# Optimization experiments

Measured on AMD Instinct MI355X. Metric: run time of the kernel, lower is better.

The kernel has to match this reference:

```python
import jax, jax.numpy as jnp
import numpy as np

B, CIN, IMG = 2, 3, 128
E, NH, WS, L, HID = 256, 8, 8, 4, 1024
HD = E // NH
SCALE = HD ** -0.5
T = WS * WS  # tokens per window


def _layernorm(x, g, b):
    m = x.mean(-1, keepdims=True)
    v = ((x - m) ** 2).mean(-1, keepdims=True)
    return (x - m) * jax.lax.rsqrt(v + 1e-5) * g + b


def _build_mask(H, W, ws, ss):
    # Swin shifted-window mask, built with static numpy (H,W,ws,ss are static)
    img = np.zeros((H, W), np.float32)
    cnt = 0
    sl = lambda n: (slice(0, n - ws), slice(n - ws, n - ss), slice(n - ss, n))
    for h in sl(H):
        for w in sl(W):
            img[h, w] = cnt
            cnt += 1
    mw = img.reshape(H // ws, ws, W // ws, ws).transpose(0, 2, 1, 3).reshape(-1, ws * ws)
    d = mw[:, None, :] - mw[:, :, None]
    return jnp.asarray(np.where(d != 0, -100.0, 0.0).astype(np.float32))  # [nW,T,T]


def _win_attn(xseq, H, W, wqkv, bqkv, wproj, bproj, mask):
    Bn, N, C = xseq.shape
    nWh, nWw = H // WS, W // WS
    nW = nWh * nWw
    # window partition: [B,N,C] -> [B*nW, T, C]
    xw = xseq.reshape(Bn, nWh, WS, nWw, WS, C).transpose(0, 1, 3, 2, 4, 5).reshape(Bn * nW, T, C)
    qkv = (xw @ wqkv + bqkv).reshape(Bn * nW, T, 3, NH, HD).transpose(2, 0, 3, 1, 4)
    q, k, v = qkv[0], qkv[1], qkv[2]  # [B*nW, NH, T, HD]
    attn = jnp.einsum('whtd,whsd->whts', q, k) * SCALE
    if mask is not None:
        attn = (attn.reshape(Bn, nW, NH, T, T) + mask[None, :, None]).reshape(Bn * nW, NH, T, T)
    attn = jax.nn.softmax(attn, axis=-1)
    out = jnp.einsum('whts,whsd->wthd', attn, v).reshape(Bn * nW, T, C)
    out = out @ wproj + bproj
    # window merge
    out = out.reshape(Bn, nWh, nWw, WS, WS, C).transpose(0, 1, 3, 2, 4, 5).reshape(Bn, H * W, C)
    return out


def _forward(x, in_w, in_b, pos, ln1_g, ln1_b, qkv_w, qkv_b, proj_w, proj_b,
             ln2_g, ln2_b, mlp_w1, mlp_b1, mlp_w2, mlp_b2, out_w, out_b):
    Bx, _, H, W = x.shape
    ss = WS // 2
    y = jnp.einsum('bchw,ec->behw', x, in_w) + in_b[None, :, None, None] + pos
    seq = y.transpose(0, 2, 3, 1).reshape(Bx, H * W, E)
    mask = _build_mask(H, W, WS, ss)
    for i in range(L):
        shifted = (i % 2 == 1)
        if shifted:
            seq = jnp.roll(seq.reshape(Bx, H, W, E), (-ss, -ss), (1, 2)).reshape(Bx, H * W, E)
        h = _layernorm(seq, ln1_g[i], ln1_b[i])
        seq = seq + _win_attn(h, H, W, qkv_w[i], qkv_b[i], proj_w[i], proj_b[i],
                              mask if shifted else None)
        h = _layernorm(seq, ln2_g[i], ln2_b[i])
        seq = seq + (jax.nn.gelu(h @ mlp_w1[i] + mlp_b1[i], approximate=False) @ mlp_w2[i] + mlp_b2[i])
        if shifted:
            seq = jnp.roll(seq.reshape(Bx, H, W, E), (ss, ss), (1, 2)).reshape(Bx, H * W, E)
    out = seq.reshape(Bx, H, W, E).transpose(0, 3, 1, 2)
    return jnp.einsum('bchw,ec->behw', out, out_w) + out_b[None, :, None, None]


def setup_inputs() -> dict:
    key = jax.random.key(0)
    ks = jax.random.split(key, 10)
    std = jnp.float32(0.02)
    return {
        'x': jax.random.normal(ks[0], (B, CIN, IMG, IMG), jnp.float32),
        'in_w': jax.random.normal(ks[1], (E, CIN), jnp.float32) * std,
        'in_b': jnp.zeros((E,), jnp.float32),
        'pos': jax.random.normal(ks[2], (1, E, IMG, IMG), jnp.float32) * std,
        'ln1_g': jnp.ones((L, E), jnp.float32),
        'ln1_b': jnp.zeros((L, E), jnp.float32),
        'qkv_w': jax.random.normal(ks[3], (L, E, 3 * E), jnp.float32) * std,
        'qkv_b': jnp.zeros((L, 3 * E), jnp.float32),
        'proj_w': jax.random.normal(ks[4], (L, E, E), jnp.float32) * std,
        'proj_b': jnp.zeros((L, E), jnp.float32),
        'ln2_g': jnp.ones((L, E), jnp.float32),
        'ln2_b': jnp.zeros((L, E), jnp.float32),
        'mlp_w1': jax.random.normal(ks[5], (L, E, HID), jnp.float32) * std,
        'mlp_b1': jnp.zeros((L, HID), jnp.float32),
        'mlp_w2': jax.random.normal(ks[6], (L, HID, E), jnp.float32) * std,
        'mlp_b2': jnp.zeros((L, E), jnp.float32),
        'out_w': jax.random.normal(ks[7], (E, E), jnp.float32) * std,
        'out_b': jnp.zeros((E,), jnp.float32),
    }


def reference(x, in_w, in_b, pos, ln1_g, ln1_b, qkv_w, qkv_b, proj_w, proj_b,
              ln2_g, ln2_b, mlp_w1, mlp_b1, mlp_w2, mlp_b2, out_w, out_b):
    return _forward(x, in_w, in_b, pos, ln1_g, ln1_b, qkv_w, qkv_b, proj_w, proj_b,
                    ln2_g, ln2_b, mlp_w1, mlp_b1, mlp_w2, mlp_b2, out_w, out_b)
```

## Files before the change

kernel.cpp:

```cpp
#include <hip/hip_runtime.h>
#include <math.h>

#define E_DIM 256
#define NPB 16384
#define M_TOT 32768

typedef __attribute__((ext_vector_type(4))) float f32x4;
typedef __attribute__((ext_vector_type(8))) short s16x8;

__device__ inline unsigned short f2bu(float f) {
  union { float f; unsigned int i; } x; x.f = f;
  unsigned int r = x.i + 0x7fffu + ((x.i >> 16) & 1u);
  return (unsigned short)(r >> 16);
}
__device__ inline float bu2f(unsigned short u) {
  union { unsigned int i; float f; } x; x.i = ((unsigned int)u) << 16; return x.f;
}
__device__ inline void gload16(const void* g, void* l) {
  __builtin_amdgcn_global_load_lds(
      (const __attribute__((address_space(1))) void*)g,
      (__attribute__((address_space(3))) void*)l, 16, 0, 0);
}
__device__ inline float fgelu(float v) {
  float u2 = 2.0f * v * (0.7978845608f + 0.0356774081f * v * v);
  u2 = fminf(fmaxf(u2, -30.0f), 30.0f);
  float e = __expf(u2);
  return v * (e / (e + 1.0f));
}

__global__ __launch_bounds__(256) void embed_kernel(
    const float* __restrict__ x, const float* __restrict__ in_w,
    const float* __restrict__ in_b, const float* __restrict__ pos,
    float* __restrict__ seq)
{
  __shared__ float ld[32][33];
  int e0 = blockIdx.x * 32;
  int n0 = blockIdx.y * 32;
  int b  = n0 >> 14;
  int np = n0 & (NPB - 1);
  int tx = threadIdx.x & 31, ty = threadIdx.x >> 5;
  #pragma unroll
  for (int i = 0; i < 4; i++)
    ld[ty + 8*i][tx] = pos[(size_t)(e0 + ty + 8*i) * NPB + np + tx];
  __syncthreads();
  #pragma unroll
  for (int i = 0; i < 4; i++) {
    int n = np + ty + 8*i;
    float x0 = x[(b*3 + 0)*NPB + n];
    float x1 = x[(b*3 + 1)*NPB + n];
    float x2 = x[(b*3 + 2)*NPB + n];
    int e = e0 + tx;
    float v = x0*in_w[e*3+0] + x1*in_w[e*3+1] + x2*in_w[e*3+2] + in_b[e]
            + ld[tx][ty + 8*i];
    seq[(size_t)(n0 + ty + 8*i) * E_DIM + e] = v;
  }
}

__global__ __launch_bounds__(256) void ln_kernel(
    const float* __restrict__ x, const float* __restrict__ g,
    const float* __restrict__ b, unsigned short* __restrict__ y)
{
  int token = blockIdx.x * 4 + (threadIdx.x >> 6);
  int lane  = threadIdx.x & 63;
  const float4* xr = (const float4*)(x + (size_t)token * E_DIM);
  float4 v = xr[lane];
  float s = v.x + v.y + v.z + v.w;
  #pragma unroll
  for (int off = 32; off; off >>= 1) s += __shfl_xor(s, off);
  float mean = s * (1.0f / E_DIM);
  float d0 = v.x - mean, d1 = v.y - mean, d2 = v.z - mean, d3 = v.w - mean;
  float q = d0*d0 + d1*d1 + d2*d2 + d3*d3;
  #pragma unroll
  for (int off = 32; off; off >>= 1) q += __shfl_xor(q, off);
  float rstd = rsqrtf(q * (1.0f / E_DIM) + 1e-5f);
  float4 gg = ((const float4*)g)[lane];
  float4 bb = ((const float4*)b)[lane];
  ushort4 o;
  o.x = f2bu(d0 * rstd * gg.x + bb.x);
  o.y = f2bu(d1 * rstd * gg.y + bb.y);
  o.z = f2bu(d2 * rstd * gg.z + bb.z);
  o.w = f2bu(d3 * rstd * gg.w + bb.w);
  *(ushort4*)(y + (size_t)token * E_DIM + lane * 4) = o;
}

__global__ __launch_bounds__(256) void wconv_t(
    const float* __restrict__ W, unsigned short* __restrict__ Wt, int K, int N)
{
  __shared__ float t[32][33];
  int nb = blockIdx.x * 32, kb = blockIdx.y * 32;
  int tx = threadIdx.x & 31, ty = threadIdx.x >> 5;
  #pragma unroll
  for (int i = 0; i < 32; i += 8)
    t[ty + i][tx] = W[(size_t)(kb + ty + i) * N + nb + tx];
  __syncthreads();
  #pragma unroll
  for (int i = 0; i < 32; i += 8)
    Wt[(size_t)(nb + ty + i) * K + kb + tx] = f2bu(t[tx][ty + i]);
}

__global__ __launch_bounds__(256) void bconv(
    const float* __restrict__ a, unsigned short* __restrict__ o, int n)
{
  int i = blockIdx.x * 1024 + threadIdx.x * 4;
  float4 v = *(const float4*)(a + i);
  ushort4 u; u.x = f2bu(v.x); u.y = f2bu(v.y); u.z = f2bu(v.z); u.w = f2bu(v.w);
  *(ushort4*)(o + i) = u;
}

__device__ inline int rowf(int r) { return (r & 3) ^ ((r >> 2) & 3); }

template<int ACT, int OCHW, int OBF>
__global__ __launch_bounds__(512) void mgemm_a(
    const unsigned short* __restrict__ A, const unsigned short* __restrict__ Wt,
    const float* __restrict__ bias, void* __restrict__ Cv, int N, int K)
{
  __shared__ unsigned short Al[2][128 * 32];
  __shared__ unsigned short Bl[2][256 * 32];
  const int tid  = threadIdx.x;
  const int lane = tid & 63;
  const int wid  = tid >> 6;
  const int wr = wid >> 2, wc = wid & 3;
  const int nbx = N >> 8;
  const int bid = blockIdx.x;
  const int lt  = (bid & 7) * ((int)gridDim.x >> 3) + (bid >> 3);
  const int bn  = (lt % nbx) * 256, bm = (lt / nbx) * 128;

  f32x4 acc[4][4];
  #pragma unroll
  for (int m = 0; m < 4; m++)
    #pragma unroll
    for (int n = 0; n < 4; n++)
      acc[m][n] = (f32x4){0.f, 0.f, 0.f, 0.f};

  const int srow = tid >> 2;
  const int cs   = (tid & 3) ^ rowf(srow);
  const unsigned short* aSrc  = A  + (size_t)(bm + srow) * K + cs * 8;
  const unsigned short* bSrc0 = Wt + (size_t)(bn + srow) * K + cs * 8;
  const unsigned short* bSrc1 = Wt + (size_t)(bn + srow + 128) * K + cs * 8;

  const int slotx = (lane >> 4) ^ (lane & 3) ^ ((lane >> 2) & 3);
  const int aoff = (wr*64 + (lane & 15)) * 64 + slotx * 16;
  const int boff = (wc*64 + (lane & 15)) * 64 + slotx * 16;

  {
    gload16(aSrc,  (char*)Al[0] + tid * 16);
    gload16(bSrc0, (char*)Bl[0] + tid * 16);
    gload16(bSrc1, (char*)Bl[0] + tid * 16 + 8192);
  }
  __syncthreads();

  const int nt = K >> 5;
  int cur = 0;
  for (int t = 0; t < nt; ++t) {
    if (t + 1 < nt) {
      int k0 = (t + 1) << 5;
      gload16(aSrc + k0,  (char*)Al[cur ^ 1] + tid * 16);
      gload16(bSrc0 + k0, (char*)Bl[cur ^ 1] + tid * 16);
      gload16(bSrc1 + k0, (char*)Bl[cur ^ 1] + tid * 16 + 8192);
    }
    const char* ab = (const char*)Al[cur] + aoff;
    const char* bb = (const char*)Bl[cur] + boff;
    s16x8 af[4], bf_[4];
    #pragma unroll
    for (int m = 0; m < 4; m++) af[m]  = *(const s16x8*)(ab + m * 1024);
    #pragma unroll
    for (int n = 0; n < 4; n++) bf_[n] = *(const s16x8*)(bb + n * 1024);
    #pragma unroll
    for (int m = 0; m < 4; m++)
      #pragma unroll
      for (int n = 0; n < 4; n++)
        acc[m][n] = __builtin_amdgcn_mfma_f32_16x16x32_bf16(af[m], bf_[n], acc[m][n], 0, 0, 0);
    __syncthreads();
    cur ^= 1;
  }

  float bv[4];
  #pragma unroll
  for (int n = 0; n < 4; n++) bv[n] = bias[bn + wc*64 + n*16 + (lane & 15)];

  #pragma unroll
  for (int m = 0; m < 4; m++) {
    int row0 = bm + wr*64 + m*16 + (lane >> 4) * 4;
    #pragma unroll
    for (int n = 0; n < 4; n++) {
      int col = bn + wc*64 + n*16 + (lane & 15);
      if (OCHW) {
        int bb2 = row0 >> 14, n0 = row0 & (NPB - 1);
        float4 st;
        st.x = acc[m][n][0] + bv[n]; st.y = acc[m][n][1] + bv[n];
        st.z = acc[m][n][2] + bv[n]; st.w = acc[m][n][3] + bv[n];
        *(float4*)((float*)Cv + (size_t)bb2 * E_DIM * NPB + (size_t)col * NPB + n0) = st;
      } else {
        #pragma unroll
        for (int j = 0; j < 4; j++) {
          int row = row0 + j;
          float v = acc[m][n][j] + bv[n];
          if (ACT) v = fgelu(v);
          if (OBF) ((unsigned short*)Cv)[(size_t)row * N + col] = f2bu(v);
          else     ((float*)Cv)[(size_t)row * N + col] = v;
        }
      }
    }
  }
}

template<int LNC>
__global__ __launch_bounds__(512) void mgemm_res(
    const unsigned short* __restrict__ A, const unsigned short* __restrict__ Wt,
    const float* __restrict__ bias, float* __restrict__ seq,
    const float* __restrict__ gamma, const float* __restrict__ beta,
    unsigned short* __restrict__ hb, int K)
{
  __shared__ unsigned short Al[2][64 * 32];
  __shared__ unsigned short Bl[2][256 * 32];
  __shared__ float2 ws[64][4];
  const int tid  = threadIdx.x;
  const int lane = tid & 63;
  const int wid  = tid >> 6;
  const int wr = wid >> 2, wc = wid & 3;
  const int bid = blockIdx.x;
  const int lt  = (bid & 7) * ((int)gridDim.x >> 3) + (bid >> 3);
  const int bm  = lt * 64;

  f32x4 acc[2][4];
  #pragma unroll
  for (int m = 0; m < 2; m++)
    #pragma unroll
    for (int n = 0; n < 4; n++)
      acc[m][n] = (f32x4){0.f, 0.f, 0.f, 0.f};

  const int srow = tid >> 2;
  const int cs   = (tid & 3) ^ rowf(srow);
  const unsigned short* aSrc  = A  + (size_t)(bm + srow) * K + cs * 8;
  const unsigned short* bSrc0 = Wt + (size_t)srow * K + cs * 8;
  const unsigned short* bSrc1 = Wt + (size_t)(srow + 128) * K + cs * 8;

  const int slotx = (lane >> 4) ^ (lane & 3) ^ ((lane >> 2) & 3);
  const int aoff = (wr*32 + (lane & 15)) * 64 + slotx * 16;
  const int boff = (wc*64 + (lane & 15)) * 64 + slotx * 16;

  {
    if (tid < 256) gload16(aSrc, (char*)Al[0] + tid * 16);
    gload16(bSrc0, (char*)Bl[0] + tid * 16);
    gload16(bSrc1, (char*)Bl[0] + tid * 16 + 8192);
  }
  __syncthreads();

  const int nt = K >> 5;
  int cur = 0;
  for (int t = 0; t < nt; ++t) {
    if (t + 1 < nt) {
      int k0 = (t + 1) << 5;
      if (tid < 256) gload16(aSrc + k0, (char*)Al[cur ^ 1] + tid * 16);
      gload16(bSrc0 + k0, (char*)Bl[cur ^ 1] + tid * 16);
      gload16(bSrc1 + k0, (char*)Bl[cur ^ 1] + tid * 16 + 8192);
    }
    const char* ab = (const char*)Al[cur] + aoff;
    const char* bb = (const char*)Bl[cur] + boff;
    s16x8 af[2], bf_[4];
    #pragma unroll
    for (int m = 0; m < 2; m++) af[m]  = *(const s16x8*)(ab + m * 1024);
    #pragma unroll
    for (int n = 0; n < 4; n++) bf_[n] = *(const s16x8*)(bb + n * 1024);
    #pragma unroll
    for (int m = 0; m < 2; m++)
      #pragma unroll
      for (int n = 0; n < 4; n++)
        acc[m][n] = __builtin_amdgcn_mfma_f32_16x16x32_bf16(af[m], bf_[n], acc[m][n], 0, 0, 0);
    __syncthreads();
    cur ^= 1;
  }

  const int lc = lane & 15, lg = lane >> 4;
  float bv[4], gv[4], btv[4];
  #pragma unroll
  for (int n = 0; n < 4; n++) {
    int col = wc*64 + n*16 + lc;
    bv[n] = bias[col];
    if (LNC) { gv[n] = gamma[col]; btv[n] = beta[col]; }
  }

  #pragma unroll
  for (int m = 0; m < 2; m++)
    #pragma unroll
    for (int j = 0; j < 4; j++) {
      int row = bm + wr*32 + m*16 + lg*4 + j;
      #pragma unroll
      for (int n = 0; n < 4; n++) {
        int col = wc*64 + n*16 + lc;
        float v = acc[m][n][j] + bv[n] + seq[(size_t)row * 256 + col];
        seq[(size_t)row * 256 + col] = v;
        acc[m][n][j] = v;
      }
    }

  if (LNC) {
    #pragma unroll
    for (int m = 0; m < 2; m++)
      #pragma unroll
      for (int j = 0; j < 4; j++) {
        float s = acc[m][0][j] + acc[m][1][j] + acc[m][2][j] + acc[m][3][j];
        float q = acc[m][0][j]*acc[m][0][j] + acc[m][1][j]*acc[m][1][j]
                + acc[m][2][j]*acc[m][2][j] + acc[m][3][j]*acc[m][3][j];
        s += __shfl_xor(s, 1); q += __shfl_xor(q, 1);
        s += __shfl_xor(s, 2); q += __shfl_xor(q, 2);
        s += __shfl_xor(s, 4); q += __shfl_xor(q, 4);
        s += __shfl_xor(s, 8); q += __shfl_xor(q, 8);
        if (lc == 0) ws[wr*32 + m*16 + lg*4 + j][wc] = (float2){s, q};
      }
    __syncthreads();
  }

  #pragma unroll
  for (int m = 0; m < 2; m++)
    #pragma unroll
    for (int j = 0; j < 4; j++) {
      int r = wr*32 + m*16 + lg*4 + j;
      float mean = 0.f, rstd = 1.f;
      if (LNC) {
        float2 a0 = ws[r][0], a1 = ws[r][1], a2 = ws[r][2], a3 = ws[r][3];
        float s = a0.x + a1.x + a2.x + a3.x;
        float q = a0.y + a1.y + a2.y + a3.y;
        mean = s * (1.0f / 256.0f);
        rstd = rsqrtf(q * (1.0f / 256.0f) - mean * mean + 1e-5f);
      }
      unsigned short* hrow = hb + (size_t)(bm + r) * 256;
      #pragma unroll
      for (int n = 0; n < 4; n++) {
        int col = wc*64 + n*16 + lc;
        float o = LNC ? (acc[m][n][j] - mean) * rstd * gv[n] + btv[n]
                      : acc[m][n][j];
        hrow[col] = f2bu(o);
      }
    }
}

template<int SHIFT>
__global__ __launch_bounds__(256) void mattn(
    const unsigned short* __restrict__ qkv, unsigned short* __restrict__ out)
{
  __shared__ unsigned short Vt_s[4][32 * 64];
  __shared__ unsigned short Pl_s[4][64 * 64];
  const int tid = threadIdx.x, wid = tid >> 6, l = tid & 63;
  const int task = blockIdx.x * 4 + wid;
  const int head = task & 7;
  const int wf = task >> 3;
  const int b = wf >> 8, win = wf & 255;
  const int wh = win >> 4, ww = win & 15;
  unsigned short* Vt = Vt_s[wid];
  unsigned short* Pl = Pl_s[wid];
  const int lg = l >> 4, lc = l & 15;

  auto tok_of = [&](int t) -> int {
    int hs = wh * 8 + (t >> 3), ws = ww * 8 + (t & 7);
    if (SHIFT) { hs = (hs + 4) & 127; ws = (ws + 4) & 127; }
    return b * NPB + hs * 128 + ws;
  };
  auto reg_of = [&](int t) -> int {
    int hs = wh * 8 + (t >> 3), ws = ww * 8 + (t & 7);
    int a = (hs < 120) ? 0 : ((hs < 124) ? 1 : 2);
    int c = (ws < 120) ? 0 : ((ws < 124) ? 1 : 2);
    return a * 3 + c;
  };

  s16x8 qf[4], kf[4];
  #pragma unroll
  for (int m = 0; m < 4; m++) {
    const unsigned short* rp = qkv + (size_t)tok_of(m * 16 + lc) * 768 + head * 32 + lg * 8;
    qf[m] = *(const s16x8*)(rp);
    kf[m] = *(const s16x8*)(rp + 256);
  }
  {
    const unsigned short* vp = qkv + (size_t)tok_of(l) * 768 + 512 + head * 32;
    #pragma unroll
    for (int d8 = 0; d8 < 4; d8++) {
      s16x8 vv = *(const s16x8*)(vp + d8 * 8);
      #pragma unroll
      for (int j = 0; j < 8; j++) {
        int d = d8 * 8 + j;
        Vt[(d * 64 + l) ^ ((d & 7) << 3)] = (unsigned short)vv[j];
      }
    }
  }

  f32x4 sT[4][4];
  #pragma unroll
  for (int m = 0; m < 4; m++)
    #pragma unroll
    for (int qt = 0; qt < 4; qt++) {
      f32x4 z = (f32x4){0.f, 0.f, 0.f, 0.f};
      sT[m][qt] = __builtin_amdgcn_mfma_f32_16x16x32_bf16(kf[m], qf[qt], z, 0, 0, 0);
    }

  int qreg[4], kreg2[16];
  if (SHIFT) {
    #pragma unroll
    for (int qt = 0; qt < 4; qt++) qreg[qt] = reg_of(qt * 16 + lc);
    #pragma unroll
    for (int m = 0; m < 4; m++)
      #pragma unroll
      for (int r = 0; r < 4; r++) kreg2[m * 4 + r] = reg_of(m * 16 + lg * 4 + r);
  }

  const float scale = 0.17677669529663687f;
  #pragma unroll
  for (int qt = 0; qt < 4; qt++) {
    float mx = -1e30f;
    #pragma unroll
    for (int m = 0; m < 4; m++)
      #pragma unroll
      for (int r = 0; r < 4; r++) {
        float s = sT[m][qt][r] * scale;
        if (SHIFT && qreg[qt] != kreg2[m * 4 + r]) s -= 100.0f;
        sT[m][qt][r] = s;
        mx = fmaxf(mx, s);
      }
    mx = fmaxf(mx, __shfl_xor(mx, 16));
    mx = fmaxf(mx, __shfl_xor(mx, 32));
    float sum = 0.f;
    #pragma unroll
    for (int m = 0; m < 4; m++)
      #pragma unroll
      for (int r = 0; r < 4; r++) {
        float p = __expf(sT[m][qt][r] - mx);
        sT[m][qt][r] = p;
        sum += p;
      }
    sum += __shfl_xor(sum, 16);
    sum += __shfl_xor(sum, 32);
    float inv = 1.0f / sum;
    int q = qt * 16 + lc;
    #pragma unroll
    for (int m = 0; m < 4; m++) {
      ushort4 pk;
      pk.x = f2bu(sT[m][qt][0] * inv);
      pk.y = f2bu(sT[m][qt][1] * inv);
      pk.z = f2bu(sT[m][qt][2] * inv);
      pk.w = f2bu(sT[m][qt][3] * inv);
      *(ushort4*)(Pl + ((q * 64 + m * 16 + lg * 4) ^ ((q & 7) << 3))) = pk;
    }
  }

  f32x4 oacc[4][2];
  #pragma unroll
  for (int qt = 0; qt < 4; qt++)
    #pragma unroll
    for (int n = 0; n < 2; n++)
      oacc[qt][n] = (f32x4){0.f, 0.f, 0.f, 0.f};
  #pragma unroll
  for (int kb = 0; kb < 2; kb++) {
    s16x8 pa[4], vb[2];
    #pragma unroll
    for (int qt = 0; qt < 4; qt++) {
      int q = qt * 16 + lc;
      pa[qt] = *(const s16x8*)(Pl + ((q * 64 + kb * 32 + lg * 8) ^ ((q & 7) << 3)));
    }
    #pragma unroll
    for (int n = 0; n < 2; n++) {
      int d = n * 16 + lc;
      vb[n] = *(const s16x8*)(Vt + ((d * 64 + kb * 32 + lg * 8) ^ ((d & 7) << 3)));
    }
    #pragma unroll
    for (int qt = 0; qt < 4; qt++)
      #pragma unroll
      for (int n = 0; n < 2; n++)
        oacc[qt][n] = __builtin_amdgcn_mfma_f32_16x16x32_bf16(pa[qt], vb[n], oacc[qt][n], 0, 0, 0);
  }

  #pragma unroll
  for (int qt = 0; qt < 4; qt++)
    #pragma unroll
    for (int r = 0; r < 4; r++) {
      int q = qt * 16 + lg * 4 + r;
      unsigned short* ob = out + (size_t)tok_of(q) * 256 + head * 32;
      ob[lc]      = f2bu(oacc[qt][0][r]);
      ob[16 + lc] = f2bu(oacc[qt][1][r]);
    }
}

extern "C" void kernel_launch(void* const* d_in, const int* in_sizes, int n_in,
                              void* d_out, int out_size, void* d_ws, size_t ws_size,
                              hipStream_t stream) {
  (void)in_sizes; (void)n_in; (void)out_size; (void)ws_size;
  const float* x      = (const float*)d_in[0];
  const float* in_w   = (const float*)d_in[1];
  const float* in_b   = (const float*)d_in[2];
  const float* pos    = (const float*)d_in[3];
  const float* ln1_g  = (const float*)d_in[4];
  const float* ln1_b  = (const float*)d_in[5];
  const float* qkv_w  = (const float*)d_in[6];
  const float* qkv_b  = (const float*)d_in[7];
  const float* proj_w = (const float*)d_in[8];
  const float* proj_b = (const float*)d_in[9];
  const float* ln2_g  = (const float*)d_in[10];
  const float* ln2_b  = (const float*)d_in[11];
  const float* mlp_w1 = (const float*)d_in[12];
  const float* mlp_b1 = (const float*)d_in[13];
  const float* mlp_w2 = (const float*)d_in[14];
  const float* mlp_b2 = (const float*)d_in[15];
  const float* out_w  = (const float*)d_in[16];
  const float* out_b  = (const float*)d_in[17];
  float* outp = (float*)d_out;

  char* p = (char*)d_ws;
  float* seq = (float*)p;                 p += (size_t)M_TOT * E_DIM * 4;
  unsigned short* bigb = (unsigned short*)p; p += (size_t)M_TOT * 1024 * 2;
  unsigned short* hb = (unsigned short*)p;   p += (size_t)M_TOT * E_DIM * 2;
  unsigned short* wb = (unsigned short*)p;
  unsigned short* qkvT = wb;
  unsigned short* projT = qkvT + 4 * 768 * 256;
  unsigned short* w1T   = projT + 4 * 256 * 256;
  unsigned short* w2T   = w1T   + 4 * 1024 * 256;
  unsigned short* outwb = w2T   + 4 * 256 * 1024;

  for (int i = 0; i < 4; i++) {
    wconv_t<<<dim3(24, 8),  256, 0, stream>>>(qkv_w  + (size_t)i*256*768,  qkvT + (size_t)i*768*256,  256, 768);
    wconv_t<<<dim3(8, 8),   256, 0, stream>>>(proj_w + (size_t)i*256*256,  projT+ (size_t)i*256*256,  256, 256);
    wconv_t<<<dim3(32, 8),  256, 0, stream>>>(mlp_w1 + (size_t)i*256*1024, w1T  + (size_t)i*1024*256, 256, 1024);
    wconv_t<<<dim3(8, 32),  256, 0, stream>>>(mlp_w2 + (size_t)i*1024*256, w2T  + (size_t)i*256*1024, 1024, 256);
  }
  bconv<<<64, 256, 0, stream>>>(out_w, outwb, 65536);

  embed_kernel<<<dim3(8, 1024), 256, 0, stream>>>(x, in_w, in_b, pos, seq);
  ln_kernel<<<8192, 256, 0, stream>>>(seq, ln1_g, ln1_b, hb);

  for (int i = 0; i < 4; i++) {
    int shifted = i & 1;
    mgemm_a<0,0,1><<<768, 512, 0, stream>>>(
        hb, qkvT + (size_t)i*768*256, qkv_b + i*768, bigb, 768, 256);
    if (shifted) mattn<1><<<1024, 256, 0, stream>>>(bigb, hb);
    else         mattn<0><<<1024, 256, 0, stream>>>(bigb, hb);
    mgemm_res<1><<<512, 512, 0, stream>>>(
        hb, projT + (size_t)i*256*256, proj_b + i*256, seq,
        ln2_g + i*256, ln2_b + i*256, hb, 256);
    mgemm_a<1,0,1><<<1024, 512, 0, stream>>>(
        hb, w1T + (size_t)i*1024*256, mlp_b1 + i*1024, bigb, 1024, 256);
    if (i < 3)
      mgemm_res<1><<<512, 512, 0, stream>>>(
          bigb, w2T + (size_t)i*256*1024, mlp_b2 + i*256, seq,
          ln1_g + (i+1)*256, ln1_b + (i+1)*256, hb, 1024);
    else
      mgemm_res<0><<<512, 512, 0, stream>>>(
          bigb, w2T + (size_t)i*256*1024, mlp_b2 + i*256, seq,
          nullptr, nullptr, hb, 1024);
  }

  mgemm_a<0,1,0><<<256, 512, 0, stream>>>(
      hb, outwb, out_b, outp, 256, 256);
}
```

Measured before the change: 642.2 us.

## Triple-buffer LDS in GEMM with prefetch depth two and vmcnt waits

Moves the bf16 GEMM's shared-memory staging from double to triple buffering. Loads are issued two K-tiles ahead, and a partial s_waitcnt vmcnt replaces the full __syncthreads, with a single barrier per iteration. The aim is to hide global-to-LDS latency better and drop one barrier per tile. LDS use grows from 48KB to 72KB per block, which may reduce occupancy, and correctness depends on the hand-placed waitcnt counts and barrier ordering.

New measurement: 638.5 us. No clear change (-0.6%).

```diff
diff --git a/kernel.cpp b/kernel.cpp
--- a/kernel.cpp
+++ b/kernel.cpp
@@ -114,8 +114,8 @@
     const unsigned short* __restrict__ A, const unsigned short* __restrict__ Wt,
     const float* __restrict__ bias, void* __restrict__ Cv, int N, int K)
 {
-  __shared__ unsigned short Al[2][128 * 32];
-  __shared__ unsigned short Bl[2][256 * 32];
+  __shared__ unsigned short Al[3][128 * 32];
+  __shared__ unsigned short Bl[3][256 * 32];
   const int tid  = threadIdx.x;
   const int lane = tid & 63;
   const int wid  = tid >> 6;
@@ -142,24 +142,25 @@
   const int aoff = (wr*64 + (lane & 15)) * 64 + slotx * 16;
   const int boff = (wc*64 + (lane & 15)) * 64 + slotx * 16;
 
-  {
-    gload16(aSrc,  (char*)Al[0] + tid * 16);
-    gload16(bSrc0, (char*)Bl[0] + tid * 16);
-    gload16(bSrc1, (char*)Bl[0] + tid * 16 + 8192);
-  }
-  __syncthreads();
+  auto STAGE = [&](int buf, int t) {
+    int k0 = t << 5;
+    gload16(aSrc + k0,  (char*)Al[buf] + tid * 16);
+    gload16(bSrc0 + k0, (char*)Bl[buf] + tid * 16);
+    gload16(bSrc1 + k0, (char*)Bl[buf] + tid * 16 + 8192);
+  };
+
+  STAGE(0, 0); STAGE(1, 1);
 
   const int nt = K >> 5;
-  int cur = 0;
   for (int t = 0; t < nt; ++t) {
-    if (t + 1 < nt) {
-      int k0 = (t + 1) << 5;
-      gload16(aSrc + k0,  (char*)Al[cur ^ 1] + tid * 16);
-      gload16(bSrc0 + k0, (char*)Bl[cur ^ 1] + tid * 16);
-      gload16(bSrc1 + k0, (char*)Bl[cur ^ 1] + tid * 16 + 8192);
-    }
-    const char* ab = (const char*)Al[cur] + aoff;
-    const char* bb = (const char*)Bl[cur] + boff;
+    if (t + 1 < nt) asm volatile("s_waitcnt vmcnt(3)" ::: "memory");
+    else            asm volatile("s_waitcnt vmcnt(0)" ::: "memory");
+    __builtin_amdgcn_s_barrier();
+    asm volatile("" ::: "memory");
+    if (t + 2 < nt) STAGE((t + 2) % 3, t + 2);
+
+    const char* ab = (const char*)Al[t % 3] + aoff;
+    const char* bb = (const char*)Bl[t % 3] + boff;
     s16x8 af[4], bf_[4];
     #pragma unroll
     for (int m = 0; m < 4; m++) af[m]  = *(const s16x8*)(ab + m * 1024);
@@ -170,8 +171,6 @@
       #pragma unroll
       for (int n = 0; n < 4; n++)
         acc[m][n] = __builtin_amdgcn_mfma_f32_16x16x32_bf16(af[m], bf_[n], acc[m][n], 0, 0, 0);
-    __syncthreads();
-    cur ^= 1;
   }
 
   float bv[4];
```

## Permute MLP hidden dimension so fc1 epilogue writes packed 8-byte bf16 stores

Applied to the files above, without the earlier changes.

The fc1 GEMM epilogue now writes four adjacent bf16 values per row as one ushort4 store, instead of scattered 2-byte stores. The hidden columns therefore land in a permuted order within each 64-column group. To keep the result correct, the fc2 weight conversion permutes its K index the same way, so the contraction over the hidden dimension is unchanged. This cuts store transactions in the fc1 epilogue, at the cost of a coupled layout convention between two kernels.

Result: no change. 647.3 us (+0.8%).

```diff
diff --git a/kernel.cpp b/kernel.cpp
--- a/kernel.cpp
+++ b/kernel.cpp
@@ -83,6 +83,7 @@
   *(ushort4*)(y + (size_t)token * E_DIM + lane * 4) = o;
 }
 
+template<int KPERM>
 __global__ __launch_bounds__(256) void wconv_t(
     const float* __restrict__ W, unsigned short* __restrict__ Wt, int K, int N)
 {
@@ -94,8 +95,11 @@
     t[ty + i][tx] = W[(size_t)(kb + ty + i) * N + nb + tx];
   __syncthreads();
   #pragma unroll
-  for (int i = 0; i < 32; i += 8)
-    Wt[(size_t)(nb + ty + i) * K + kb + tx] = f2bu(t[tx][ty + i]);
+  for (int i = 0; i < 32; i += 8) {
+    int k = kb + tx;
+    int ko = KPERM ? ((k & ~63) | ((k & 15) << 2) | ((k >> 4) & 3)) : k;
+    Wt[(size_t)(nb + ty + i) * K + ko] = f2bu(t[tx][ty + i]);
+  }
 }
 
 __global__ __launch_bounds__(256) void bconv(
@@ -109,7 +113,7 @@
 
 __device__ inline int rowf(int r) { return (r & 3) ^ ((r >> 2) & 3); }
 
-template<int ACT, int OCHW, int OBF>
+template<int ACT, int OCHW, int OBF, int PERM>
 __global__ __launch_bounds__(512) void mgemm_a(
     const unsigned short* __restrict__ A, const unsigned short* __restrict__ Wt,
     const float* __restrict__ bias, void* __restrict__ Cv, int N, int K)
@@ -177,6 +181,26 @@
   float bv[4];
   #pragma unroll
   for (int n = 0; n < 4; n++) bv[n] = bias[bn + wc*64 + n*16 + (lane & 15)];
+
+  if (OBF && PERM) {
+    #pragma unroll
+    for (int m = 0; m < 4; m++) {
+      int row0 = bm + wr*64 + m*16 + (lane >> 4) * 4;
+      #pragma unroll
+      for (int j = 0; j < 4; j++) {
+        int row = row0 + j;
+        ushort4 pk;
+        float v0 = acc[m][0][j] + bv[0];
+        float v1 = acc[m][1][j] + bv[1];
+        float v2 = acc[m][2][j] + bv[2];
+        float v3 = acc[m][3][j] + bv[3];
+        if (ACT) { v0 = fgelu(v0); v1 = fgelu(v1); v2 = fgelu(v2); v3 = fgelu(v3); }
+        pk.x = f2bu(v0); pk.y = f2bu(v1); pk.z = f2bu(v2); pk.w = f2bu(v3);
+        *(ushort4*)((unsigned short*)Cv + (size_t)row * N + bn + wc*64 + (lane & 15) * 4) = pk;
+      }
+    }
+    return;
+  }
 
   #pragma unroll
   for (int m = 0; m < 4; m++) {
@@ -514,10 +538,10 @@
   unsigned short* outwb = w2T   + 4 * 256 * 1024;
 
   for (int i = 0; i < 4; i++) {
-    wconv_t<<<dim3(24, 8),  256, 0, stream>>>(qkv_w  + (size_t)i*256*768,  qkvT + (size_t)i*768*256,  256, 768);
-    wconv_t<<<dim3(8, 8),   256, 0, stream>>>(proj_w + (size_t)i*256*256,  projT+ (size_t)i*256*256,  256, 256);
-    wconv_t<<<dim3(32, 8),  256, 0, stream>>>(mlp_w1 + (size_t)i*256*1024, w1T  + (size_t)i*1024*256, 256, 1024);
-    wconv_t<<<dim3(8, 32),  256, 0, stream>>>(mlp_w2 + (size_t)i*1024*256, w2T  + (size_t)i*256*1024, 1024, 256);
+    wconv_t<0><<<dim3(24, 8),  256, 0, stream>>>(qkv_w  + (size_t)i*256*768,  qkvT + (size_t)i*768*256,  256, 768);
+    wconv_t<0><<<dim3(8, 8),   256, 0, stream>>>(proj_w + (size_t)i*256*256,  projT+ (size_t)i*256*256,  256, 256);
+    wconv_t<0><<<dim3(32, 8),  256, 0, stream>>>(mlp_w1 + (size_t)i*256*1024, w1T  + (size_t)i*1024*256, 256, 1024);
+    wconv_t<1><<<dim3(8, 32),  256, 0, stream>>>(mlp_w2 + (size_t)i*1024*256, w2T  + (size_t)i*256*1024, 1024, 256);
   }
   bconv<<<64, 256, 0, stream>>>(out_w, outwb, 65536);
 
@@ -526,14 +550,14 @@
 
   for (int i = 0; i < 4; i++) {
     int shifted = i & 1;
-    mgemm_a<0,0,1><<<768, 512, 0, stream>>>(
+    mgemm_a<0,0,1,0><<<768, 512, 0, stream>>>(
         hb, qkvT + (size_t)i*768*256, qkv_b + i*768, bigb, 768, 256);
     if (shifted) mattn<1><<<1024, 256, 0, stream>>>(bigb, hb);
     else         mattn<0><<<1024, 256, 0, stream>>>(bigb, hb);
     mgemm_res<1><<<512, 512, 0, stream>>>(
         hb, projT + (size_t)i*256*256, proj_b + i*256, seq,
         ln2_g + i*256, ln2_b + i*256, hb, 256);
-    mgemm_a<1,0,1><<<1024, 512, 0, stream>>>(
+    mgemm_a<1,0,1,1><<<1024, 512, 0, stream>>>(
         hb, w1T + (size_t)i*1024*256, mlp_b1 + i*1024, bigb, 1024, 256);
     if (i < 3)
       mgemm_res<1><<<512, 512, 0, stream>>>(
@@ -545,6 +569,6 @@
           nullptr, nullptr, hb, 1024);
   }
 
-  mgemm_a<0,1,0><<<256, 512, 0, stream>>>(
+  mgemm_a<0,1,0,0><<<256, 512, 0, stream>>>(
       hb, outwb, out_b, outp, 256, 256);
 }
```
